# Kernel tuning notes

Hardware: AMD Instinct MI355X
Metric: run time of the kernel (lower is better)

## Reference

```python
import jax, jax.numpy as jnp
import numpy as np

B, C, D = 65536, 10, 18
V, N, E = 100000, 99999, 128
EPS = 1e-9


def setup_inputs() -> dict:
    key = jax.random.key(0)
    k1, k2, k3, k4, k5 = jax.random.split(key, 5)
    return {
        "context_idxs": jax.random.randint(k1, (B, C), 0, V, dtype=jnp.int32),
        "path_nodes": jax.random.randint(k2, (B, D), 0, N, dtype=jnp.int32),
        "codes": jax.random.randint(k3, (B, D), 0, 2, dtype=jnp.int32),
        "in_embed": jax.random.normal(k4, (V, E), dtype=jnp.float32),
        "node_embed": jax.random.normal(k5, (N, E), dtype=jnp.float32),
    }


def reference(context_idxs, path_nodes, codes, in_embed, node_embed):
    # v: mean of context word embeddings -> [B, E]
    v = in_embed[context_idxs].mean(axis=1)
    # u: embeddings of internal tree nodes along the Huffman path -> [B, D, E]
    u = node_embed[path_nodes]
    # logits along the path: u . v -> [B, D]
    logits = jnp.einsum("bde,be->bd", u, v)
    s = jax.nn.sigmoid(logits)
    # p = s if code==1 else 1-s ; loss = -sum log(p + eps) per example
    p = jnp.where(codes == 1, s, 1.0 - s)
    loss = -jnp.sum(jnp.log(p + EPS), axis=1)  # [B]
    return loss
```

## Files before the change

### kernel.cpp

```cpp
#include <hip/hip_runtime.h>
#include <math.h>


constexpr int Bn = 65536;
constexpr int Cn = 10;
constexpr int Dn = 18;
constexpr float EPS = 1e-9f;

__global__ __launch_bounds__(256) void cbow_hs_kernel(
    const int* __restrict__ ctx,
    const int* __restrict__ nodes,
    const int* __restrict__ codes,
    const float* __restrict__ in_embed,
    const float* __restrict__ node_embed,
    float* __restrict__ out)
{
    const int wave = threadIdx.x >> 6;
    const int lane = threadIdx.x & 63;
    const int sl   = lane & 31;
    const bool hi  = lane >= 32;
    const int b = (blockIdx.x << 2) + wave;

    int cidx[Cn];
    const int2* c2 = (const int2*)(ctx + b * Cn);
    #pragma unroll
    for (int k = 0; k < Cn / 2; ++k) {
        int2 t = c2[k]; cidx[2 * k] = t.x; cidx[2 * k + 1] = t.y;
    }
    int nidx[Dn];
    const int2* n2 = (const int2*)(nodes + b * Dn);
    #pragma unroll
    for (int k = 0; k < Dn / 2; ++k) {
        int2 t = n2[k]; nidx[2 * k] = t.x; nidx[2 * k + 1] = t.y;
    }

    const float4* __restrict__ in4 = (const float4*)in_embed;
    const float4* __restrict__ ne4 = (const float4*)node_embed;

    float4 vs = make_float4(0.f, 0.f, 0.f, 0.f);
    #pragma unroll
    for (int c = 0; c < Cn; c += 2) {
        int idx = hi ? cidx[c + 1] : cidx[c];
        float4 e = in4[(size_t)idx * 32 + sl];
        vs.x += e.x; vs.y += e.y; vs.z += e.z; vs.w += e.w;
    }
    vs.x += __shfl_xor(vs.x, 32, 64);
    vs.y += __shfl_xor(vs.y, 32, 64);
    vs.z += __shfl_xor(vs.z, 32, 64);
    vs.w += __shfl_xor(vs.w, 32, 64);
    float4 v;
    v.x = vs.x * (1.0f / Cn); v.y = vs.y * (1.0f / Cn);
    v.z = vs.z * (1.0f / Cn); v.w = vs.w * (1.0f / Cn);

    float pd[Dn / 2];
    #pragma unroll
    for (int i = 0; i < Dn / 2; ++i) {
        int idx = hi ? nidx[2 * i + 1] : nidx[2 * i];
        float4 u = ne4[(size_t)idx * 32 + sl];
        pd[i] = u.x * v.x + u.y * v.y + u.z * v.z + u.w * v.w;
    }

    #pragma unroll
    for (int i = 0; i < Dn / 2; ++i) {
        #pragma unroll
        for (int m = 16; m >= 1; m >>= 1)
            pd[i] += __shfl_xor(pd[i], m, 64);
    }

    float myv = 0.f;
    #pragma unroll
    for (int i = 0; i < Dn / 2; ++i)
        myv = (sl == i) ? pd[i] : myv;

    const int d  = 2 * sl + (hi ? 1 : 0);
    const int cd = codes[b * Dn + ((sl < Dn / 2) ? d : 0)];

    float s = 1.0f / (1.0f + expf(-myv));
    float p = (cd == 1) ? s : 1.0f - s;
    float t = (sl < Dn / 2) ? -logf(p + EPS) : 0.f;

    #pragma unroll
    for (int m = 32; m >= 1; m >>= 1)
        t += __shfl_xor(t, m, 64);

    if (lane == 0) out[b] = t;
}

extern "C" void kernel_launch(void* const* d_in, const int* in_sizes, int n_in,
                              void* d_out, int out_size, void* d_ws, size_t ws_size,
                              hipStream_t stream) {
    const int*   ctx        = (const int*)d_in[0];
    const int*   path_nodes = (const int*)d_in[1];
    const int*   codes      = (const int*)d_in[2];
    const float* in_embed   = (const float*)d_in[3];
    const float* node_embed = (const float*)d_in[4];
    float*       out        = (float*)d_out;

    dim3 grid(Bn / 4);
    dim3 block(256);
    cbow_hs_kernel<<<grid, block, 0, stream>>>(ctx, path_nodes, codes,
                                               in_embed, node_embed, out);
}
```

Measured before the change: 232.8 us.

## Issue all embedding gathers upfront and make index loads wave-uniform scalar

All context and path-node embedding rows are loaded into registers before any arithmetic, so all 14 gathers are in flight at once and the node gathers no longer wait on the v reduction. The wave index goes through readfirstlane, which makes the index loads uniform so they can become scalar loads, and address math uses 32-bit unsigned shifts. Launch bounds ask for 6 blocks per CU to hold occupancy despite the extra registers the buffered float4s need.

```diff
diff --git a/kernel.cpp b/kernel.cpp
--- a/kernel.cpp
+++ b/kernel.cpp
@@ -7,7 +7,7 @@
 constexpr int Dn = 18;
 constexpr float EPS = 1e-9f;
 
-__global__ __launch_bounds__(256) void cbow_hs_kernel(
+__global__ __launch_bounds__(256, 6) void cbow_hs_kernel(
     const int* __restrict__ ctx,
     const int* __restrict__ nodes,
     const int* __restrict__ codes,
@@ -15,34 +15,39 @@
     const float* __restrict__ node_embed,
     float* __restrict__ out)
 {
-    const int wave = threadIdx.x >> 6;
+    const int wv   = __builtin_amdgcn_readfirstlane(threadIdx.x >> 6);
     const int lane = threadIdx.x & 63;
     const int sl   = lane & 31;
     const bool hi  = lane >= 32;
-    const int b = (blockIdx.x << 2) + wave;
+    const int b    = (blockIdx.x << 2) + wv;
 
     int cidx[Cn];
-    const int2* c2 = (const int2*)(ctx + b * Cn);
     #pragma unroll
-    for (int k = 0; k < Cn / 2; ++k) {
-        int2 t = c2[k]; cidx[2 * k] = t.x; cidx[2 * k + 1] = t.y;
-    }
+    for (int c = 0; c < Cn; ++c) cidx[c] = ctx[b * Cn + c];
     int nidx[Dn];
-    const int2* n2 = (const int2*)(nodes + b * Dn);
     #pragma unroll
-    for (int k = 0; k < Dn / 2; ++k) {
-        int2 t = n2[k]; nidx[2 * k] = t.x; nidx[2 * k + 1] = t.y;
-    }
+    for (int d = 0; d < Dn; ++d) nidx[d] = nodes[b * Dn + d];
 
     const float4* __restrict__ in4 = (const float4*)in_embed;
     const float4* __restrict__ ne4 = (const float4*)node_embed;
 
+    float4 ce[Cn / 2];
+    #pragma unroll
+    for (int k = 0; k < Cn / 2; ++k) {
+        unsigned idx = (unsigned)(hi ? cidx[2 * k + 1] : cidx[2 * k]);
+        ce[k] = in4[(idx << 5) + sl];
+    }
+    float4 ue[Dn / 2];
+    #pragma unroll
+    for (int i = 0; i < Dn / 2; ++i) {
+        unsigned idx = (unsigned)(hi ? nidx[2 * i + 1] : nidx[2 * i]);
+        ue[i] = ne4[(idx << 5) + sl];
+    }
+
     float4 vs = make_float4(0.f, 0.f, 0.f, 0.f);
     #pragma unroll
-    for (int c = 0; c < Cn; c += 2) {
-        int idx = hi ? cidx[c + 1] : cidx[c];
-        float4 e = in4[(size_t)idx * 32 + sl];
-        vs.x += e.x; vs.y += e.y; vs.z += e.z; vs.w += e.w;
+    for (int k = 0; k < Cn / 2; ++k) {
+        vs.x += ce[k].x; vs.y += ce[k].y; vs.z += ce[k].z; vs.w += ce[k].w;
     }
     vs.x += __shfl_xor(vs.x, 32, 64);
     vs.y += __shfl_xor(vs.y, 32, 64);
@@ -54,11 +59,8 @@
 
     float pd[Dn / 2];
     #pragma unroll
-    for (int i = 0; i < Dn / 2; ++i) {
-        int idx = hi ? nidx[2 * i + 1] : nidx[2 * i];
-        float4 u = ne4[(size_t)idx * 32 + sl];
-        pd[i] = u.x * v.x + u.y * v.y + u.z * v.z + u.w * v.w;
-    }
+    for (int i = 0; i < Dn / 2; ++i)
+        pd[i] = ue[i].x * v.x + ue[i].y * v.y + ue[i].z * v.z + ue[i].w * v.w;
 
     #pragma unroll
     for (int i = 0; i < Dn / 2; ++i) {
```

Result: no change. 233.5 us (+0.3%).
